# Performance work log

Hardware: AMD Instinct MI355X
Metric: run time of the kernel (lower is better)

The kernel has to match this reference:

```python
import jax, jax.numpy as jnp
import numpy as np

DIM = 256
HEADS = 8
HEAD_DIM = DIM // HEADS
EPS = 1e-5


def layer_norm(x, g, b):
    mu = jnp.mean(x, axis=-1, keepdims=True)
    var = jnp.mean(jnp.square(x - mu), axis=-1, keepdims=True)
    return (x - mu) * jax.lax.rsqrt(var + EPS) * g + b


def setup_inputs() -> dict:
    key = jax.random.key(0)
    ks = jax.random.split(key, 10)
    s = 0.02
    return {
        "x": jax.random.normal(ks[0], (4, DIM, 64, 64), dtype=jnp.float32),
        "g1": jnp.ones((DIM,), jnp.float32),
        "b1": jnp.zeros((DIM,), jnp.float32),
        "Wqkv": jax.random.normal(ks[1], (DIM, 3 * DIM), jnp.float32) * s,
        "Wp": jax.random.normal(ks[2], (DIM, DIM), jnp.float32) * s,
        "bp": jnp.zeros((DIM,), jnp.float32),
        "g2": jnp.ones((DIM,), jnp.float32),
        "b2": jnp.zeros((DIM,), jnp.float32),
        "W1": jax.random.normal(ks[3], (DIM, 2 * DIM), jnp.float32) * s,
        "bf1": jnp.zeros((2 * DIM,), jnp.float32),
        "W2": jax.random.normal(ks[4], (2 * DIM, DIM), jnp.float32) * s,
        "bf2": jnp.zeros((DIM,), jnp.float32),
    }


def reference(x, g1, b1, Wqkv, Wp, bp, g2, b2, W1, bf1, W2, bf2):
    B, C, H, W = x.shape
    N = H * W
    scale = HEAD_DIM ** -0.5
    tokens = x.reshape(B, C, N).transpose(0, 2, 1)  # [B,N,C]
    t = layer_norm(tokens, g1, b1)
    qkv = (t @ Wqkv).reshape(B, N, 3, HEADS, HEAD_DIM)
    q = qkv[:, :, 0].transpose(0, 2, 1, 3)  # [B,h,N,d]
    k = qkv[:, :, 1].transpose(0, 2, 1, 3)
    v = qkv[:, :, 2].transpose(0, 2, 1, 3)
    attn = jax.nn.softmax(jnp.einsum("bhnd,bhmd->bhnm", q, k) * scale, axis=-1)
    out = jnp.einsum("bhnm,bhmd->bhnd", attn, v)
    out = out.transpose(0, 2, 1, 3).reshape(B, N, C)
    tokens = tokens + out @ Wp + bp
    t2 = layer_norm(tokens, g2, b2)
    h = jax.nn.gelu(t2 @ W1 + bf1, approximate=False)
    tokens = tokens + h @ W2 + bf2
    return tokens.transpose(0, 2, 1).reshape(B, C, H, W)
```

## Files before the change

### kernel.cpp

```cpp
#include <hip/hip_runtime.h>

typedef unsigned short u16;
typedef unsigned int   u32;

using bf16x8 = __attribute__((ext_vector_type(8))) __bf16;
using f32x4  = __attribute__((ext_vector_type(4))) float;
using f32x16 = __attribute__((ext_vector_type(16))) float;

#define MFMA16(a, b, c) __builtin_amdgcn_mfma_f32_16x16x32_bf16((a), (b), (c), 0, 0, 0)
#define MFMA32(a, b, c) __builtin_amdgcn_mfma_f32_32x32x16_bf16((a), (b), (c), 0, 0, 0)

__device__ inline u16 f2bf(float f) {
  u32 x = __float_as_uint(f);
  return (u16)((x + 0x7FFFu + ((x >> 16) & 1u)) >> 16);
}

__device__ inline const bf16x8* bfp(const u16* p) {
  return reinterpret_cast<const bf16x8*>(p);
}

__global__ __launch_bounds__(256) void k_conv(
    const float* __restrict__ Wqkv, const float* __restrict__ Wp,
    const float* __restrict__ W1,   const float* __restrict__ W2,
    u16* __restrict__ wqkvT, u16* __restrict__ wpT,
    u16* __restrict__ w1T,   u16* __restrict__ w2T) {
  __shared__ float tile[32][33];
  int blk = blockIdx.x;
  const float* src; u16* dst; int R, C, t;
  if (blk < 192)      { src = Wqkv; dst = wqkvT; R = 256; C = 768; t = blk; }
  else if (blk < 256) { src = Wp;   dst = wpT;   R = 256; C = 256; t = blk - 192; }
  else if (blk < 384) { src = W1;   dst = w1T;   R = 256; C = 512; t = blk - 256; }
  else                { src = W2;   dst = w2T;   R = 512; C = 256; t = blk - 384; }
  int tpc = C >> 5;
  int tr = (t / tpc) << 5, tc = (t % tpc) << 5;
  int j = threadIdx.x & 31, iq = threadIdx.x >> 5;
  #pragma unroll
  for (int i = 0; i < 4; ++i)
    tile[iq + 8 * i][j] = src[(size_t)(tr + iq + 8 * i) * C + tc + j];
  __syncthreads();
  #pragma unroll
  for (int i = 0; i < 4; ++i)
    dst[(size_t)(tc + iq + 8 * i) * R + tr + j] = f2bf(tile[j][iq + 8 * i]);
}

__global__ __launch_bounds__(256) void k_ln1(
    const float* __restrict__ x, const float* __restrict__ g1,
    const float* __restrict__ b1, float* __restrict__ tokens,
    u16* __restrict__ ln) {
  __shared__ float tile[256][33];
  __shared__ float red[2][8][32];
  __shared__ float stat[2][32];
  int tid = threadIdx.x;
  int blk = blockIdx.x;
  int b = blk >> 7, n0 = (blk & 127) << 5;
  {
    int cq = tid >> 5, j = tid & 31;
    const float* xp = x + (((size_t)b * 256) << 12) + n0 + j;
    #pragma unroll 8
    for (int it = 0; it < 32; ++it) {
      int c = it * 8 + cq;
      tile[c][j] = xp[(size_t)c << 12];
    }
  }
  __syncthreads();
  {
    int tn = tid & 31, qq = tid >> 5;
    float s = 0.f, s2 = 0.f;
    #pragma unroll 8
    for (int i = 0; i < 32; ++i) {
      float v = tile[qq * 32 + i][tn];
      s += v; s2 += v * v;
    }
    red[0][qq][tn] = s; red[1][qq][tn] = s2;
  }
  __syncthreads();
  if (tid < 32) {
    float su = 0.f, sq = 0.f;
    #pragma unroll
    for (int qq = 0; qq < 8; ++qq) { su += red[0][qq][tid]; sq += red[1][qq][tid]; }
    float mu  = su * (1.f / 256.f);
    float var = sq * (1.f / 256.f) - mu * mu;
    stat[0][tid] = mu;
    stat[1][tid] = rsqrtf(var + 1e-5f);
  }
  __syncthreads();
  float g = g1[tid], bb = b1[tid];
  size_t base = ((size_t)(b * 4096 + n0)) * 256 + tid;
  for (int it = 0; it < 32; ++it) {
    float v = tile[tid][it];
    float y = (v - stat[0][it]) * stat[1][it] * g + bb;
    tokens[base + (size_t)it * 256] = v;
    ln[base + (size_t)it * 256] = f2bf(y);
  }
}

template <int K>
__device__ inline void mm16(const u16* __restrict__ A, const u16* __restrict__ BT,
                            int arow, int bcol, f32x4 acc[4]) {
  int lane = threadIdx.x & 63;
  int r = lane & 15, g = lane >> 4;
  const u16* ap  = A  + (size_t)(arow + r) * K + g * 8;
  const u16* bp0 = BT + (size_t)(bcol + r) * K + g * 8;
  #pragma unroll 4
  for (int k0 = 0; k0 < K; k0 += 32) {
    bf16x8 a = *bfp(ap + k0);
    #pragma unroll
    for (int nt = 0; nt < 4; ++nt) {
      bf16x8 b = *bfp(bp0 + nt * 16 * K + k0);
      acc[nt] = MFMA16(a, b, acc[nt]);
    }
  }
}

template <int K>
__device__ inline void mm32(const u16* __restrict__ A, const u16* __restrict__ BT,
                            int arow, int bcol, f32x4 acc[2][4]) {
  int lane = threadIdx.x & 63;
  int r = lane & 15, g = lane >> 4;
  const u16* ap0 = A  + (size_t)(arow + r) * K + g * 8;
  const u16* bp0 = BT + (size_t)(bcol + r) * K + g * 8;
  #pragma unroll 4
  for (int k0 = 0; k0 < K; k0 += 32) {
    bf16x8 a0 = *bfp(ap0 + k0);
    bf16x8 a1 = *bfp(ap0 + 16 * K + k0);
    #pragma unroll
    for (int nt = 0; nt < 4; ++nt) {
      bf16x8 b = *bfp(bp0 + nt * 16 * K + k0);
      acc[0][nt] = MFMA16(a0, b, acc[0][nt]);
      acc[1][nt] = MFMA16(a1, b, acc[1][nt]);
    }
  }
}

__global__ __launch_bounds__(256) void k_qkv(
    const u16* __restrict__ ln, const u16* __restrict__ wT,
    u16* __restrict__ q, u16* __restrict__ kf, u16* __restrict__ vf) {
  int w = threadIdx.x >> 6, lane = threadIdx.x & 63;
  int r16 = lane & 15, g4 = lane >> 4;
  int m0 = blockIdx.y * 128 + w * 32;
  int n0 = blockIdx.x * 64;
  f32x4 z = {0.f, 0.f, 0.f, 0.f};
  f32x4 acc[2][4] = {{z, z, z, z}, {z, z, z, z}};
  mm32<256>(ln, wT, m0, n0, acc);
  int b = m0 >> 12;
  const float qs = (float)(0.17677669529663687 * 1.4426950408889634);
  #pragma unroll
  for (int rg = 0; rg < 2; ++rg) {
    int nbase = (m0 & 4095) + rg * 16 + g4 * 4;
    #pragma unroll
    for (int nt = 0; nt < 4; ++nt) {
      int col = n0 + nt * 16 + r16;
      int which = col >> 8, h = (col >> 5) & 7, d = col & 31;
      size_t bh_off = ((size_t)(b * 8 + h)) << 17;
      if (which == 0) {
        #pragma unroll
        for (int r = 0; r < 4; ++r)
          q[((size_t)(b * 8 + h) * 4096 + nbase + r) * 32 + d] =
              f2bf(acc[rg][nt][r] * qs);
      } else if (which == 1) {
        int sel = d >> 4, lh = (d >> 3) & 1, jj = d & 7;
        #pragma unroll
        for (int r = 0; r < 4; ++r) {
          int key = nbase + r;
          kf[bh_off + (size_t)(key >> 5) * 1024 + sel * 512 +
             (((key & 31) | (lh << 5)) << 3) + jj] = f2bf(acc[rg][nt][r]);
        }
      } else {
        int kk = nbase & 31;
        int sel = kk >> 4, lh = (kk >> 3) & 1, j0 = kk & 7;
        ushort4 o4;
        o4.x = f2bf(acc[rg][nt][0]); o4.y = f2bf(acc[rg][nt][1]);
        o4.z = f2bf(acc[rg][nt][2]); o4.w = f2bf(acc[rg][nt][3]);
        *(ushort4*)(vf + bh_off + (size_t)(nbase >> 5) * 1024 + sel * 512 +
                    ((d | (lh << 5)) << 3) + j0) = o4;
      }
    }
  }
}

__global__ __launch_bounds__(512, 4) void k_attn(
    const u16* __restrict__ q, const u16* __restrict__ kf,
    const u16* __restrict__ vf, u16* __restrict__ attnout) {
  __shared__ float obuf[2][3][64][17];
  __shared__ float lsbuf[2][3][64];
  int lane = threadIdx.x & 63;
  int w = threadIdx.x >> 6;
  int qi = w >> 2, kj = w & 3;
  int r32 = lane & 31, hi = lane >> 5;
  int d = blockIdx.x;
  int bh = (d & 7) + 8 * (d >> 8);
  int qt = (d >> 3) & 31;
  int q0 = qt * 128 + qi * 64;
  const u16* qh = q + ((size_t)bh << 17);
  bf16x8 qf00 = *bfp(qh + (size_t)(q0 + r32) * 32 + hi * 8);
  bf16x8 qf01 = *bfp(qh + (size_t)(q0 + r32) * 32 + 16 + hi * 8);
  bf16x8 qf10 = *bfp(qh + (size_t)(q0 + 32 + r32) * 32 + hi * 8);
  bf16x8 qf11 = *bfp(qh + (size_t)(q0 + 32 + r32) * 32 + 16 + hi * 8);

  const u16* kp = kf + ((size_t)bh << 17) + (size_t)kj * 32768 + lane * 8;
  const u16* vp = vf + ((size_t)bh << 17) + (size_t)kj * 32768 + lane * 8;

  f32x16 o0, o1, zz;
  #pragma unroll
  for (int r = 0; r < 16; ++r) { o0[r] = 0.f; o1[r] = 0.f; zz[r] = 0.f; }
  float ls0 = 0.f, ls1 = 0.f;

  #pragma unroll 2
  for (int c = 0; c < 32; ++c) {
    bf16x8 ka0 = *bfp(kp);
    bf16x8 ka1 = *bfp(kp + 512);
    bf16x8 va0 = *bfp(vp);
    bf16x8 va1 = *bfp(vp + 512);
    kp += 1024; vp += 1024;

    {
      f32x16 s = MFMA32(ka0, qf00, zz);
      s = MFMA32(ka1, qf01, s);
      #pragma unroll
      for (int r = 0; r < 16; ++r) s[r] = __builtin_amdgcn_exp2f(s[r]);
      float t0 = ((s[0] + s[1]) + (s[2] + s[3])) + ((s[4] + s[5]) + (s[6] + s[7]));
      float t1 = ((s[8] + s[9]) + (s[10] + s[11])) + ((s[12] + s[13]) + (s[14] + s[15]));
      ls0 += t0 + t1;
      u32 c8[8];
      #pragma unroll
      for (int i = 0; i < 8; ++i)
        asm("v_cvt_pk_bf16_f32 %0, %1, %2" : "=v"(c8[i]) : "v"(s[2 * i]), "v"(s[2 * i + 1]));
      asm("v_permlane32_swap_b32 %0, %1" : "+v"(c8[0]), "+v"(c8[2]));
      asm("v_permlane32_swap_b32 %0, %1" : "+v"(c8[1]), "+v"(c8[3]));
      asm("v_permlane32_swap_b32 %0, %1" : "+v"(c8[4]), "+v"(c8[6]));
      asm("v_permlane32_swap_b32 %0, %1" : "+v"(c8[5]), "+v"(c8[7]));
      union { u32 u[4]; bf16x8 v; } pf0, pf1;
      pf0.u[0] = c8[0]; pf0.u[1] = c8[1]; pf0.u[2] = c8[2]; pf0.u[3] = c8[3];
      pf1.u[0] = c8[4]; pf1.u[1] = c8[5]; pf1.u[2] = c8[6]; pf1.u[3] = c8[7];
      o0 = MFMA32(va0, pf0.v, o0);
      o0 = MFMA32(va1, pf1.v, o0);
    }
    {
      f32x16 s = MFMA32(ka0, qf10, zz);
      s = MFMA32(ka1, qf11, s);
      #pragma unroll
      for (int r = 0; r < 16; ++r) s[r] = __builtin_amdgcn_exp2f(s[r]);
      float t0 = ((s[0] + s[1]) + (s[2] + s[3])) + ((s[4] + s[5]) + (s[6] + s[7]));
      float t1 = ((s[8] + s[9]) + (s[10] + s[11])) + ((s[12] + s[13]) + (s[14] + s[15]));
      ls1 += t0 + t1;
      u32 c8[8];
      #pragma unroll
      for (int i = 0; i < 8; ++i)
        asm("v_cvt_pk_bf16_f32 %0, %1, %2" : "=v"(c8[i]) : "v"(s[2 * i]), "v"(s[2 * i + 1]));
      asm("v_permlane32_swap_b32 %0, %1" : "+v"(c8[0]), "+v"(c8[2]));
      asm("v_permlane32_swap_b32 %0, %1" : "+v"(c8[1]), "+v"(c8[3]));
      asm("v_permlane32_swap_b32 %0, %1" : "+v"(c8[4]), "+v"(c8[6]));
      asm("v_permlane32_swap_b32 %0, %1" : "+v"(c8[5]), "+v"(c8[7]));
      union { u32 u[4]; bf16x8 v; } pf0, pf1;
      pf0.u[0] = c8[0]; pf0.u[1] = c8[1]; pf0.u[2] = c8[2]; pf0.u[3] = c8[3];
      pf1.u[0] = c8[4]; pf1.u[1] = c8[5]; pf1.u[2] = c8[6]; pf1.u[3] = c8[7];
      o1 = MFMA32(va0, pf0.v, o1);
      o1 = MFMA32(va1, pf1.v, o1);
    }
  }

  ls0 += __shfl_xor(ls0, 32);
  ls1 += __shfl_xor(ls1, 32);

  if (kj != 0) {
    #pragma unroll
    for (int g = 0; g < 16; ++g) obuf[qi][kj - 1][lane][g] = o0[g];
    lsbuf[qi][kj - 1][lane] = ls0;
  }
  __syncthreads();
  float inv0 = 0.f;
  if (kj == 0) {
    float lst = ls0 + lsbuf[qi][0][lane] + lsbuf[qi][1][lane] + lsbuf[qi][2][lane];
    inv0 = __builtin_amdgcn_rcpf(lst);
    #pragma unroll
    for (int g = 0; g < 16; ++g)
      o0[g] += obuf[qi][0][lane][g] + obuf[qi][1][lane][g] + obuf[qi][2][lane][g];
  }
  __syncthreads();
  if (kj != 0) {
    #pragma unroll
    for (int g = 0; g < 16; ++g) obuf[qi][kj - 1][lane][g] = o1[g];
    lsbuf[qi][kj - 1][lane] = ls1;
  }
  __syncthreads();
  if (kj == 0) {
    int b = bh >> 3, h = bh & 7;
    float lst1 = ls1 + lsbuf[qi][0][lane] + lsbuf[qi][1][lane] + lsbuf[qi][2][lane];
    float inv1 = __builtin_amdgcn_rcpf(lst1);
    #pragma unroll
    for (int g = 0; g < 16; ++g)
      o1[g] += obuf[qi][0][lane][g] + obuf[qi][1][lane][g] + obuf[qi][2][lane][g];
    size_t nrow0 = ((size_t)(b * 4096 + q0 + r32)) * 256 + h * 32;
    size_t nrow1 = ((size_t)(b * 4096 + q0 + 32 + r32)) * 256 + h * 32;
    #pragma unroll
    for (int g = 0; g < 4; ++g) {
      ushort4 ov;
      ov.x = f2bf(o0[g * 4 + 0] * inv0);
      ov.y = f2bf(o0[g * 4 + 1] * inv0);
      ov.z = f2bf(o0[g * 4 + 2] * inv0);
      ov.w = f2bf(o0[g * 4 + 3] * inv0);
      *(ushort4*)(attnout + nrow0 + g * 8 + hi * 4) = ov;
      ushort4 ow;
      ow.x = f2bf(o1[g * 4 + 0] * inv1);
      ow.y = f2bf(o1[g * 4 + 1] * inv1);
      ow.z = f2bf(o1[g * 4 + 2] * inv1);
      ow.w = f2bf(o1[g * 4 + 3] * inv1);
      *(ushort4*)(attnout + nrow1 + g * 8 + hi * 4) = ow;
    }
  }
}

__global__ __launch_bounds__(256) void k_projln(
    const u16* __restrict__ ao, const u16* __restrict__ wT,
    const float* __restrict__ bp, const float* __restrict__ g2,
    const float* __restrict__ b2, float* __restrict__ tokens,
    u16* __restrict__ ln) {
  __shared__ float red[2][4][32];
  int w = threadIdx.x >> 6, lane = threadIdx.x & 63;
  int r16 = lane & 15, g4 = lane >> 4;
  int m0 = blockIdx.x * 32;
  int n0 = w * 64;
  f32x4 z = {0.f, 0.f, 0.f, 0.f};
  f32x4 acc[2][4] = {{z, z, z, z}, {z, z, z, z}};
  mm32<256>(ao, wT, m0, n0, acc);
  float sum[2][4], sq[2][4];
  #pragma unroll
  for (int rg = 0; rg < 2; ++rg)
    #pragma unroll
    for (int r = 0; r < 4; ++r) { sum[rg][r] = 0.f; sq[rg][r] = 0.f; }
  #pragma unroll
  for (int rg = 0; rg < 2; ++rg) {
    #pragma unroll
    for (int nt = 0; nt < 4; ++nt) {
      int col = n0 + nt * 16 + r16;
      float bias = bp[col];
      #pragma unroll
      for (int r = 0; r < 4; ++r) {
        float v = tokens[(size_t)(m0 + rg * 16 + g4 * 4 + r) * 256 + col] +
                  acc[rg][nt][r] + bias;
        acc[rg][nt][r] = v;
        sum[rg][r] += v; sq[rg][r] += v * v;
      }
    }
  }
  #pragma unroll
  for (int mask = 1; mask < 16; mask <<= 1) {
    #pragma unroll
    for (int rg = 0; rg < 2; ++rg)
      #pragma unroll
      for (int r = 0; r < 4; ++r) {
        sum[rg][r] += __shfl_xor(sum[rg][r], mask);
        sq[rg][r]  += __shfl_xor(sq[rg][r], mask);
      }
  }
  if (r16 == 0) {
    #pragma unroll
    for (int rg = 0; rg < 2; ++rg)
      #pragma unroll
      for (int r = 0; r < 4; ++r) {
        red[0][w][rg * 16 + g4 * 4 + r] = sum[rg][r];
        red[1][w][rg * 16 + g4 * 4 + r] = sq[rg][r];
      }
  }
  __syncthreads();
  #pragma unroll
  for (int rg = 0; rg < 2; ++rg) {
    float mu[4], rs[4];
    #pragma unroll
    for (int r = 0; r < 4; ++r) {
      int ri = rg * 16 + g4 * 4 + r;
      float S  = red[0][0][ri] + red[0][1][ri] + red[0][2][ri] + red[0][3][ri];
      float SQ = red[1][0][ri] + red[1][1][ri] + red[1][2][ri] + red[1][3][ri];
      mu[r] = S * (1.f / 256.f);
      rs[r] = rsqrtf(SQ * (1.f / 256.f) - mu[r] * mu[r] + 1e-5f);
    }
    #pragma unroll
    for (int nt = 0; nt < 4; ++nt) {
      int col = n0 + nt * 16 + r16;
      float gg = g2[col], bb = b2[col];
      #pragma unroll
      for (int r = 0; r < 4; ++r) {
        size_t idx = (size_t)(m0 + rg * 16 + g4 * 4 + r) * 256 + col;
        float v = acc[rg][nt][r];
        tokens[idx] = v;
        ln[idx] = f2bf((v - mu[r]) * rs[r] * gg + bb);
      }
    }
  }
}

__global__ __launch_bounds__(512) void k_mlp(
    const u16* __restrict__ ln, const u16* __restrict__ w1T,
    const float* __restrict__ bf1, const u16* __restrict__ w2T,
    const float* __restrict__ bf2, const float* __restrict__ tokens,
    float* __restrict__ out) {
  __shared__ u16 hh[32][520];
  int w = threadIdx.x >> 6, lane = threadIdx.x & 63;
  int r16 = lane & 15, g4 = lane >> 4;
  int rh = w & 1, cg = w >> 1;
  int m0 = blockIdx.x * 32 + rh * 16;
  {
    f32x4 z = {0.f, 0.f, 0.f, 0.f};
    f32x4 acc[8] = {z, z, z, z, z, z, z, z};
    const u16* ap  = ln  + (size_t)(m0 + r16) * 256 + g4 * 8;
    const u16* bp0 = w1T + (size_t)(cg * 128 + r16) * 256 + g4 * 8;
    #pragma unroll 2
    for (int k0 = 0; k0 < 256; k0 += 32) {
      bf16x8 a = *bfp(ap + k0);
      #pragma unroll
      for (int nt = 0; nt < 8; ++nt) {
        bf16x8 b = *bfp(bp0 + nt * 16 * 256 + k0);
        acc[nt] = MFMA16(a, b, acc[nt]);
      }
    }
    int rl = rh * 16 + g4 * 4;
    #pragma unroll
    for (int nt = 0; nt < 8; ++nt) {
      int col = cg * 128 + nt * 16 + r16;
      float bias = bf1[col];
      #pragma unroll
      for (int r = 0; r < 4; ++r) {
        float xx = acc[nt][r] + bias;
        float x2 = xx * xx;
        float zt = xx * (2.3021188f + 0.10293855f * x2);
        float e  = __builtin_amdgcn_exp2f(zt);
        float ge = xx * (1.f - __builtin_amdgcn_rcpf(1.f + e));
        hh[rl + r][col] = f2bf(ge);
      }
    }
  }
  __syncthreads();
  f32x4 z = {0.f, 0.f, 0.f, 0.f};
  f32x4 acc[4] = {z, z, z, z};
  const u16* hrow = &hh[rh * 16 + r16][g4 * 8];
  const u16* bp2  = w2T + (size_t)(cg * 64 + r16) * 512 + g4 * 8;
  #pragma unroll 4
  for (int k0 = 0; k0 < 512; k0 += 32) {
    bf16x8 a = *bfp(hrow + k0);
    #pragma unroll
    for (int nt = 0; nt < 4; ++nt) {
      bf16x8 b = *bfp(bp2 + nt * 16 * 512 + k0);
      acc[nt] = MFMA16(a, b, acc[nt]);
    }
  }
  int b = m0 >> 12;
  int nl = (m0 & 4095) + g4 * 4;
  #pragma unroll
  for (int nt = 0; nt < 4; ++nt) {
    int col = cg * 64 + nt * 16 + r16;
    float bias = bf2[col];
    float4 o;
    o.x = tokens[(size_t)(m0 + g4 * 4 + 0) * 256 + col] + acc[nt][0] + bias;
    o.y = tokens[(size_t)(m0 + g4 * 4 + 1) * 256 + col] + acc[nt][1] + bias;
    o.z = tokens[(size_t)(m0 + g4 * 4 + 2) * 256 + col] + acc[nt][2] + bias;
    o.w = tokens[(size_t)(m0 + g4 * 4 + 3) * 256 + col] + acc[nt][3] + bias;
    *(float4*)(out + (((size_t)(b * 256 + col)) << 12) + nl) = o;
  }
}

extern "C" void kernel_launch(void* const* d_in, const int* in_sizes, int n_in,
                              void* d_out, int out_size, void* d_ws, size_t ws_size,
                              hipStream_t stream) {
  (void)in_sizes; (void)n_in; (void)out_size; (void)ws_size;
  const float* x    = (const float*)d_in[0];
  const float* g1   = (const float*)d_in[1];
  const float* b1   = (const float*)d_in[2];
  const float* Wqkv = (const float*)d_in[3];
  const float* Wp   = (const float*)d_in[4];
  const float* bp   = (const float*)d_in[5];
  const float* g2   = (const float*)d_in[6];
  const float* b2   = (const float*)d_in[7];
  const float* W1   = (const float*)d_in[8];
  const float* bf1  = (const float*)d_in[9];
  const float* W2   = (const float*)d_in[10];
  const float* bf2  = (const float*)d_in[11];
  float* out = (float*)d_out;

  char* ws = (char*)d_ws;
  float* tokens = (float*)(ws);
  u16* lnb      = (u16*)(ws + 16777216);
  u16* qb       = (u16*)(ws + 25165824);
  u16* kfb      = (u16*)(ws + 33554432);
  u16* vfb      = (u16*)(ws + 41943040);
  u16* aob      = (u16*)(ws + 50331648);
  u16* wqkvT    = (u16*)(ws + 67108864);
  u16* wpT      = (u16*)(ws + 67502080);
  u16* w1T      = (u16*)(ws + 67633152);
  u16* w2T      = (u16*)(ws + 67895296);

  k_conv  <<<512, 256, 0, stream>>>(Wqkv, Wp, W1, W2, wqkvT, wpT, w1T, w2T);
  k_ln1   <<<512, 256, 0, stream>>>(x, g1, b1, tokens, lnb);
  k_qkv   <<<dim3(12, 128), 256, 0, stream>>>(lnb, wqkvT, qb, kfb, vfb);
  k_attn  <<<1024, 512, 0, stream>>>(qb, kfb, vfb, aob);
  k_projln<<<512, 256, 0, stream>>>(aob, wpT, bp, g2, b2, tokens, lnb);
  k_mlp   <<<512, 512, 0, stream>>>(lnb, w1T, bf1, w2T, bf2, tokens, out);
}
```

Baseline: 225.2 us.

## Fuse weight conversion into LN1 launch and compute softmax row sums via MFMA

```diff
diff --git a/kernel.cpp b/kernel.cpp
--- a/kernel.cpp
+++ b/kernel.cpp
@@ -19,38 +19,37 @@
   return reinterpret_cast<const bf16x8*>(p);
 }
 
-__global__ __launch_bounds__(256) void k_conv(
+__global__ __launch_bounds__(256) void k_pre(
+    const float* __restrict__ x, const float* __restrict__ g1,
+    const float* __restrict__ b1, float* __restrict__ tokens,
+    u16* __restrict__ ln,
     const float* __restrict__ Wqkv, const float* __restrict__ Wp,
     const float* __restrict__ W1,   const float* __restrict__ W2,
     u16* __restrict__ wqkvT, u16* __restrict__ wpT,
     u16* __restrict__ w1T,   u16* __restrict__ w2T) {
-  __shared__ float tile[32][33];
-  int blk = blockIdx.x;
-  const float* src; u16* dst; int R, C, t;
-  if (blk < 192)      { src = Wqkv; dst = wqkvT; R = 256; C = 768; t = blk; }
-  else if (blk < 256) { src = Wp;   dst = wpT;   R = 256; C = 256; t = blk - 192; }
-  else if (blk < 384) { src = W1;   dst = w1T;   R = 256; C = 512; t = blk - 256; }
-  else                { src = W2;   dst = w2T;   R = 512; C = 256; t = blk - 384; }
-  int tpc = C >> 5;
-  int tr = (t / tpc) << 5, tc = (t % tpc) << 5;
-  int j = threadIdx.x & 31, iq = threadIdx.x >> 5;
-  #pragma unroll
-  for (int i = 0; i < 4; ++i)
-    tile[iq + 8 * i][j] = src[(size_t)(tr + iq + 8 * i) * C + tc + j];
-  __syncthreads();
-  #pragma unroll
-  for (int i = 0; i < 4; ++i)
-    dst[(size_t)(tc + iq + 8 * i) * R + tr + j] = f2bf(tile[j][iq + 8 * i]);
-}
-
-__global__ __launch_bounds__(256) void k_ln1(
-    const float* __restrict__ x, const float* __restrict__ g1,
-    const float* __restrict__ b1, float* __restrict__ tokens,
-    u16* __restrict__ ln) {
   __shared__ float tile[256][33];
   __shared__ float red[2][8][32];
   __shared__ float stat[2][32];
   int tid = threadIdx.x;
+  if (blockIdx.x >= 512) {
+    int blk = blockIdx.x - 512;
+    const float* src; u16* dst; int R, C, t;
+    if (blk < 192)      { src = Wqkv; dst = wqkvT; R = 256; C = 768; t = blk; }
+    else if (blk < 256) { src = Wp;   dst = wpT;   R = 256; C = 256; t = blk - 192; }
+    else if (blk < 384) { src = W1;   dst = w1T;   R = 256; C = 512; t = blk - 256; }
+    else                { src = W2;   dst = w2T;   R = 512; C = 256; t = blk - 384; }
+    int tpc = C >> 5;
+    int tr = (t / tpc) << 5, tc = (t % tpc) << 5;
+    int j = tid & 31, iq = tid >> 5;
+    #pragma unroll
+    for (int i = 0; i < 4; ++i)
+      tile[iq + 8 * i][j] = src[(size_t)(tr + iq + 8 * i) * C + tc + j];
+    __syncthreads();
+    #pragma unroll
+    for (int i = 0; i < 4; ++i)
+      dst[(size_t)(tc + iq + 8 * i) * R + tr + j] = f2bf(tile[j][iq + 8 * i]);
+    return;
+  }
   int blk = blockIdx.x;
   int b = blk >> 7, n0 = (blk & 127) << 5;
   {
@@ -200,6 +199,10 @@
   const u16* kp = kf + ((size_t)bh << 17) + (size_t)kj * 32768 + lane * 8;
   const u16* vp = vf + ((size_t)bh << 17) + (size_t)kj * 32768 + lane * 8;
 
+  union { u32 u[4]; bf16x8 v; } ones;
+  #pragma unroll
+  for (int i = 0; i < 4; ++i) ones.u[i] = 0x3F803F80u;
+
   f32x16 o0, o1, zz;
   #pragma unroll
   for (int r = 0; r < 16; ++r) { o0[r] = 0.f; o1[r] = 0.f; zz[r] = 0.f; }
@@ -214,13 +217,12 @@
     kp += 1024; vp += 1024;
 
     {
+      __builtin_amdgcn_s_setprio(1);
       f32x16 s = MFMA32(ka0, qf00, zz);
       s = MFMA32(ka1, qf01, s);
+      __builtin_amdgcn_s_setprio(0);
       #pragma unroll
       for (int r = 0; r < 16; ++r) s[r] = __builtin_amdgcn_exp2f(s[r]);
-      float t0 = ((s[0] + s[1]) + (s[2] + s[3])) + ((s[4] + s[5]) + (s[6] + s[7]));
-      float t1 = ((s[8] + s[9]) + (s[10] + s[11])) + ((s[12] + s[13]) + (s[14] + s[15]));
-      ls0 += t0 + t1;
       u32 c8[8];
       #pragma unroll
       for (int i = 0; i < 8; ++i)
@@ -232,17 +234,21 @@
       union { u32 u[4]; bf16x8 v; } pf0, pf1;
       pf0.u[0] = c8[0]; pf0.u[1] = c8[1]; pf0.u[2] = c8[2]; pf0.u[3] = c8[3];
       pf1.u[0] = c8[4]; pf1.u[1] = c8[5]; pf1.u[2] = c8[6]; pf1.u[3] = c8[7];
+      __builtin_amdgcn_s_setprio(1);
+      f32x16 lsc = MFMA32(ones.v, pf0.v, zz);
+      lsc = MFMA32(ones.v, pf1.v, lsc);
       o0 = MFMA32(va0, pf0.v, o0);
       o0 = MFMA32(va1, pf1.v, o0);
+      __builtin_amdgcn_s_setprio(0);
+      ls0 += lsc[0];
     }
     {
+      __builtin_amdgcn_s_setprio(1);
       f32x16 s = MFMA32(ka0, qf10, zz);
       s = MFMA32(ka1, qf11, s);
+      __builtin_amdgcn_s_setprio(0);
       #pragma unroll
       for (int r = 0; r < 16; ++r) s[r] = __builtin_amdgcn_exp2f(s[r]);
-      float t0 = ((s[0] + s[1]) + (s[2] + s[3])) + ((s[4] + s[5]) + (s[6] + s[7]));
-      float t1 = ((s[8] + s[9]) + (s[10] + s[11])) + ((s[12] + s[13]) + (s[14] + s[15]));
-      ls1 += t0 + t1;
       u32 c8[8];
       #pragma unroll
       for (int i = 0; i < 8; ++i)
@@ -254,13 +260,15 @@
       union { u32 u[4]; bf16x8 v; } pf0, pf1;
       pf0.u[0] = c8[0]; pf0.u[1] = c8[1]; pf0.u[2] = c8[2]; pf0.u[3] = c8[3];
       pf1.u[0] = c8[4]; pf1.u[1] = c8[5]; pf1.u[2] = c8[6]; pf1.u[3] = c8[7];
+      __builtin_amdgcn_s_setprio(1);
+      f32x16 lsc = MFMA32(ones.v, pf0.v, zz);
+      lsc = MFMA32(ones.v, pf1.v, lsc);
       o1 = MFMA32(va0, pf0.v, o1);
       o1 = MFMA32(va1, pf1.v, o1);
-    }
-  }
-
-  ls0 += __shfl_xor(ls0, 32);
-  ls1 += __shfl_xor(ls1, 32);
+      __builtin_amdgcn_s_setprio(0);
+      ls1 += lsc[0];
+    }
+  }
 
   if (kj != 0) {
     #pragma unroll
@@ -488,8 +496,8 @@
   u16* w1T      = (u16*)(ws + 67633152);
   u16* w2T      = (u16*)(ws + 67895296);
 
-  k_conv  <<<512, 256, 0, stream>>>(Wqkv, Wp, W1, W2, wqkvT, wpT, w1T, w2T);
-  k_ln1   <<<512, 256, 0, stream>>>(x, g1, b1, tokens, lnb);
+  k_pre   <<<1024, 256, 0, stream>>>(x, g1, b1, tokens, lnb,
+                                     Wqkv, Wp, W1, W2, wqkvT, wpT, w1T, w2T);
   k_qkv   <<<dim3(12, 128), 256, 0, stream>>>(lnb, wqkvT, qb, kfb, vfb);
   k_attn  <<<1024, 512, 0, stream>>>(qb, kfb, vfb, aob);
   k_projln<<<512, 256, 0, stream>>>(aob, wpT, bp, g2, b2, tokens, lnb);
```

Result: no change. 224.6 us (-0.3%).
